# Performance work log

Hardware: AMD Instinct MI355X
Metric: run time of the kernel (lower is better)

## Reference

```python
import math
import jax, jax.numpy as jnp
import numpy as np

D_MODEL = 1024
N_HEADS = 16
D_K = 64


def setup_inputs() -> dict:
    key = jax.random.key(0)
    ks = jax.random.split(key, 12)
    N, T = 4, 2048
    hd = N_HEADS * D_K
    s_in = 1.0 / math.sqrt(D_MODEL)
    s_hd = 1.0 / math.sqrt(hd)
    return {
        "x_k": jax.random.normal(ks[0], (N, T, D_MODEL), jnp.float32),
        "x_v": jax.random.normal(ks[1], (N, T, D_MODEL), jnp.float32),
        "x_q": jax.random.normal(ks[2], (N, T, D_MODEL), jnp.float32),
        "mask": jnp.ones((N, T), jnp.int32),
        "Wk": jax.random.normal(ks[3], (D_MODEL, hd), jnp.float32) * s_in,
        "bk": jax.random.normal(ks[4], (hd,), jnp.float32) * s_in,
        "Wv": jax.random.normal(ks[5], (D_MODEL, hd), jnp.float32) * s_in,
        "bv": jax.random.normal(ks[6], (hd,), jnp.float32) * s_in,
        "Wq": jax.random.normal(ks[7], (D_MODEL, hd), jnp.float32) * s_in,
        "bq": jax.random.normal(ks[8], (hd,), jnp.float32) * s_in,
        "Wf": jax.random.normal(ks[9], (hd, D_MODEL), jnp.float32) * s_hd,
        "bf": jax.random.normal(ks[10], (D_MODEL,), jnp.float32) * s_hd,
    }


def _split_heads(x):  # [N,T,H*D] -> [N,H,T,D]
    n, t, _ = x.shape
    return x.reshape(n, t, N_HEADS, D_K).transpose(0, 2, 1, 3)


def reference(x_k, x_v, x_q, mask, Wk, bk, Wv, bv, Wq, bq, Wf, bf):
    k = _split_heads(x_k @ Wk + bk)  # projected but (faithfully) unused in scores
    v = _split_heads(x_v @ Wv + bv)
    q = _split_heads(x_q @ Wq + bq)
    # NOTE: original code computes scores from q and v (not k) — reproduced faithfully.
    scores = jnp.einsum('nhid,nhjd->nhij', q, v) / math.sqrt(D_K)
    scores = jnp.where(mask[:, None, None, :] == 0, -jnp.inf, scores)
    weights = jax.nn.softmax(scores, axis=-1)
    A = jnp.einsum('nhij,nhjd->nhid', weights, v)  # [N,H,T,D]
    n, h, t, d = A.shape
    A = A.transpose(0, 2, 1, 3).reshape(n, t, h * d)
    return A @ Wf + bf
```

## Files before the change

### kernel.cpp

```cpp
#include <hip/hip_runtime.h>
#include <cstdint>
#include <type_traits>

typedef unsigned short u16;
typedef __attribute__((ext_vector_type(8))) short short8;
typedef __attribute__((ext_vector_type(4))) float f32x4;

#define DMODEL 1024
#define TSEQ   2048
#define NHEADS 16
#define DKH    64
#define NBATCH 4
#define MROWS  (NBATCH * TSEQ)

__device__ __forceinline__ u16 f2b(float f) {
  union { float f; unsigned int u; } c; c.f = f;
  unsigned int u = c.u;
  return (u16)((u + 0x7fffu + ((u >> 16) & 1u)) >> 16);
}

__device__ __forceinline__ void gl_lds16(const u16* g, u16* l) {
  __builtin_amdgcn_global_load_lds((const __attribute__((address_space(1))) void*)g,
                                   (__attribute__((address_space(3))) void*)l, 16, 0, 0);
}

__global__ void cvt_bf16(const float* __restrict__ in, u16* __restrict__ out) {
  int i = blockIdx.x * 256 + threadIdx.x;
  const float4* p = (const float4*)in + (long long)i * 2;
  float4 a = p[0], b = p[1];
  union { u16 s[8]; uint4 v; } pk;
  pk.s[0] = f2b(a.x); pk.s[1] = f2b(a.y); pk.s[2] = f2b(a.z); pk.s[3] = f2b(a.w);
  pk.s[4] = f2b(b.x); pk.s[5] = f2b(b.y); pk.s[6] = f2b(b.z); pk.s[7] = f2b(b.w);
  ((uint4*)out)[i] = pk.v;
}

__global__ void transpose_cvt(const float* __restrict__ in, u16* __restrict__ out) {
  __shared__ float t[32][33];
  int bx = blockIdx.x * 32, by = blockIdx.y * 32;
  int tx = threadIdx.x, ty = threadIdx.y;
  #pragma unroll
  for (int i = ty; i < 32; i += 8)
    t[i][tx] = in[(by + i) * DMODEL + bx + tx];
  __syncthreads();
  #pragma unroll
  for (int i = ty; i < 32; i += 8)
    out[(bx + i) * DMODEL + by + tx] = f2b(t[tx][i]);
}

__global__ void transpose_v(const u16* __restrict__ Vb, u16* __restrict__ VbT) {
  __shared__ u16 tl[64 * 66];
  int tb = blockIdx.x, h = blockIdx.y, nb = blockIdx.z;
  int tx = threadIdx.x, ty = threadIdx.y;
  long long src = (long long)(nb * TSEQ + tb * 64) * DMODEL + h * DKH;
  #pragma unroll
  for (int r = ty; r < 64; r += 4)
    tl[r * 66 + tx] = Vb[src + (long long)r * DMODEL + tx];
  __syncthreads();
  long long dst = (long long)((nb * NHEADS + h) * DKH) * TSEQ + tb * 64;
  #pragma unroll
  for (int r = ty; r < 64; r += 4)
    VbT[dst + (long long)r * TSEQ + tx] = tl[tx * 66 + r];
}

template <typename CT>
__global__ __launch_bounds__(256, 2)
void gemm_bias(const u16* __restrict__ A, const u16* __restrict__ Bt,
               const float* __restrict__ bias, CT* __restrict__ C) {
  __shared__ u16 As[128 * 64];
  __shared__ u16 Bs[128 * 64];

  const int tid  = threadIdx.x;
  const int bm   = blockIdx.x, bn = blockIdx.y;
  const int wv   = tid >> 6, lane = tid & 63;
  const int wm   = wv >> 1, wn = wv & 1;
  const int l15  = lane & 15, quad = lane >> 4;
  const int srow = lane >> 3;
  const int gch  = (lane & 7) ^ srow;

  f32x4 acc[4][4];
  #pragma unroll
  for (int i = 0; i < 4; ++i)
    #pragma unroll
    for (int j = 0; j < 4; ++j)
      acc[i][j] = (f32x4){0.f, 0.f, 0.f, 0.f};

  const u16* Ag = A  + (long long)(bm * 128) * DMODEL;
  const u16* Bg = Bt + (long long)(bn * 128) * DMODEL;

  for (int k0 = 0; k0 < DMODEL; k0 += 64) {
    __syncthreads();
    #pragma unroll
    for (int j = 0; j < 4; ++j) {
      int rb = wv * 32 + j * 8;
      gl_lds16(Ag + (long long)(rb + srow) * DMODEL + k0 + gch * 8, As + rb * 64);
      gl_lds16(Bg + (long long)(rb + srow) * DMODEL + k0 + gch * 8, Bs + rb * 64);
    }
    __syncthreads();
    #pragma unroll
    for (int ks = 0; ks < 2; ++ks) {
      short8 af[4], bf_[4];
      #pragma unroll
      for (int mi = 0; mi < 4; ++mi) {
        int r = wm * 64 + mi * 16 + l15;
        af[mi] = *(const short8*)(As + r * 64 + (((ks * 4 + quad) ^ (r & 7)) * 8));
      }
      #pragma unroll
      for (int ni = 0; ni < 4; ++ni) {
        int r = wn * 64 + ni * 16 + l15;
        bf_[ni] = *(const short8*)(Bs + r * 64 + (((ks * 4 + quad) ^ (r & 7)) * 8));
      }
      #pragma unroll
      for (int mi = 0; mi < 4; ++mi)
        #pragma unroll
        for (int ni = 0; ni < 4; ++ni)
          acc[mi][ni] = __builtin_amdgcn_mfma_f32_16x16x32_bf16(af[mi], bf_[ni], acc[mi][ni], 0, 0, 0);
    }
  }

  #pragma unroll
  for (int ni = 0; ni < 4; ++ni) {
    int col = bn * 128 + wn * 64 + ni * 16 + l15;
    float bvf = bias[col];
    #pragma unroll
    for (int mi = 0; mi < 4; ++mi) {
      int row0 = bm * 128 + wm * 64 + mi * 16 + quad * 4;
      #pragma unroll
      for (int r = 0; r < 4; ++r) {
        float val = acc[mi][ni][r] + bvf;
        long long idx = (long long)(row0 + r) * DMODEL + col;
        if constexpr (std::is_same_v<CT, float>) C[idx] = val;
        else                                     C[idx] = f2b(val);
      }
    }
  }
}

__global__ __launch_bounds__(256, 4)
void attn_kernel(const u16* __restrict__ Qb, const u16* __restrict__ Vb,
                 const u16* __restrict__ VbT, const int* __restrict__ mask,
                 u16* __restrict__ Ab) {
  __shared__ u16 Vs[64 * 64];
  __shared__ u16 Vts[64 * 64];
  __shared__ u16 Ps[4 * 32 * 72];
  __shared__ float Msf[64];

  const int tid  = threadIdx.x;
  const int qblk = blockIdx.x, h = blockIdx.y, nb = blockIdx.z;
  const int wv   = tid >> 6, lane = tid & 63;
  const int l15  = lane & 15, quad = lane >> 4;
  const int srow = lane >> 3, gch = (lane & 7) ^ srow;

  const int q0 = qblk * 128 + wv * 32;
  const long long rowbase = (long long)nb * TSEQ;
  const long long hd = (long long)((nb * NHEADS + h) * DKH);
  u16* psb = Ps + wv * 32 * 72;

  short8 qf[2][2];
  #pragma unroll
  for (int mi = 0; mi < 2; ++mi)
    #pragma unroll
    for (int ks = 0; ks < 2; ++ks)
      qf[mi][ks] = *(const short8*)(Qb + (rowbase + q0 + mi * 16 + l15) * DMODEL
                                    + h * DKH + ks * 32 + quad * 8);

  f32x4 of[2][4];
  #pragma unroll
  for (int mi = 0; mi < 2; ++mi)
    #pragma unroll
    for (int dt = 0; dt < 4; ++dt)
      of[mi][dt] = (f32x4){0.f, 0.f, 0.f, 0.f};
  float lsum[2] = {0.f, 0.f};

  const float SC = 0.125f * 1.44269504f;

  for (int vb = 0; vb < TSEQ / 64; ++vb) {
    __syncthreads();
    #pragma unroll
    for (int j = 0; j < 2; ++j) {
      int rb = wv * 16 + j * 8;
      gl_lds16(Vb  + (rowbase + vb * 64 + rb + srow) * DMODEL + h * DKH + gch * 8, Vs  + rb * 64);
      gl_lds16(VbT + (hd + rb + srow) * TSEQ + vb * 64 + gch * 8,                  Vts + rb * 64);
    }
    if (tid < 64) Msf[tid] = mask[nb * TSEQ + vb * 64 + tid] ? 0.f : -INFINITY;
    __syncthreads();

    f32x4 st[2][4];
    #pragma unroll
    for (int mi = 0; mi < 2; ++mi)
      #pragma unroll
      for (int tt = 0; tt < 4; ++tt)
        st[mi][tt] = (f32x4){0.f, 0.f, 0.f, 0.f};
    #pragma unroll
    for (int tt = 0; tt < 4; ++tt) {
      int r = tt * 16 + l15;
      #pragma unroll
      for (int ks = 0; ks < 2; ++ks) {
        short8 vf = *(const short8*)(Vs + r * 64 + (((ks * 4 + quad) ^ (l15 & 7)) * 8));
        #pragma unroll
        for (int mi = 0; mi < 2; ++mi)
          st[mi][tt] = __builtin_amdgcn_mfma_f32_16x16x32_bf16(vf, qf[mi][ks], st[mi][tt], 0, 0, 0);
      }
    }

    f32x4 msk[4];
    #pragma unroll
    for (int tt = 0; tt < 4; ++tt)
      msk[tt] = *(const f32x4*)(Msf + tt * 16 + quad * 4);
    #pragma unroll
    for (int mi = 0; mi < 2; ++mi) {
      float ls = 0.f;
      #pragma unroll
      for (int tt = 0; tt < 4; ++tt) {
        float p0 = __builtin_amdgcn_exp2f(__builtin_fmaf(st[mi][tt][0], SC, msk[tt][0]));
        float p1 = __builtin_amdgcn_exp2f(__builtin_fmaf(st[mi][tt][1], SC, msk[tt][1]));
        float p2 = __builtin_amdgcn_exp2f(__builtin_fmaf(st[mi][tt][2], SC, msk[tt][2]));
        float p3 = __builtin_amdgcn_exp2f(__builtin_fmaf(st[mi][tt][3], SC, msk[tt][3]));
        ls += (p0 + p1) + (p2 + p3);
        uint2 pk;
        pk.x = (unsigned)f2b(p0) | ((unsigned)f2b(p1) << 16);
        pk.y = (unsigned)f2b(p2) | ((unsigned)f2b(p3) << 16);
        *(uint2*)(psb + (mi * 16 + l15) * 72 + tt * 16 + quad * 4) = pk;
      }
      lsum[mi] += ls;
    }

    #pragma unroll
    for (int kc = 0; kc < 2; ++kc) {
      short8 pf[2];
      #pragma unroll
      for (int mi = 0; mi < 2; ++mi)
        pf[mi] = *(const short8*)(psb + (mi * 16 + l15) * 72 + kc * 32 + quad * 8);
      #pragma unroll
      for (int dt = 0; dt < 4; ++dt) {
        int r = dt * 16 + l15;
        short8 vtf = *(const short8*)(Vts + r * 64 + (((kc * 4 + quad) ^ (l15 & 7)) * 8));
        #pragma unroll
        for (int mi = 0; mi < 2; ++mi)
          of[mi][dt] = __builtin_amdgcn_mfma_f32_16x16x32_bf16(vtf, pf[mi], of[mi][dt], 0, 0, 0);
      }
    }
  }

  #pragma unroll
  for (int mi = 0; mi < 2; ++mi) {
    float l = lsum[mi];
    l += __shfl_xor(l, 16, 64);
    l += __shfl_xor(l, 32, 64);
    float inv = 1.0f / l;
    long long row = rowbase + q0 + mi * 16 + l15;
    #pragma unroll
    for (int dt = 0; dt < 4; ++dt) {
      union { u16 s[4]; uint2 v; } o;
      #pragma unroll
      for (int r = 0; r < 4; ++r) o.s[r] = f2b(of[mi][dt][r] * inv);
      *(uint2*)(Ab + row * DMODEL + h * DKH + dt * 16 + quad * 4) = o.v;
    }
  }
}

extern "C" void kernel_launch(void* const* d_in, const int* in_sizes, int n_in,
                              void* d_out, int out_size, void* d_ws, size_t ws_size,
                              hipStream_t stream) {
  const float* x_v  = (const float*)d_in[1];
  const float* x_q  = (const float*)d_in[2];
  const int*   mask = (const int*)d_in[3];
  const float* Wv   = (const float*)d_in[6];
  const float* bv   = (const float*)d_in[7];
  const float* Wq   = (const float*)d_in[8];
  const float* bq   = (const float*)d_in[9];
  const float* Wf   = (const float*)d_in[10];
  const float* bfp  = (const float*)d_in[11];

  char* w = (char*)d_ws;
  u16* WqT = (u16*)(w + 0);
  u16* WvT = (u16*)(w + (2ll << 20));
  u16* WfT = (u16*)(w + (4ll << 20));
  u16* Xq  = (u16*)(w + (6ll << 20));
  u16* Xv  = (u16*)(w + (22ll << 20));
  u16* Qb  = (u16*)(w + (38ll << 20));
  u16* Vb  = (u16*)(w + (54ll << 20));
  u16* VbT = (u16*)(w + (70ll << 20));
  u16* Ab  = Xq;

  dim3 tb(32, 8), tg(32, 32);
  transpose_cvt<<<tg, tb, 0, stream>>>(Wq, WqT);
  transpose_cvt<<<tg, tb, 0, stream>>>(Wv, WvT);
  transpose_cvt<<<tg, tb, 0, stream>>>(Wf, WfT);

  cvt_bf16<<<MROWS * DMODEL / 8 / 256, 256, 0, stream>>>(x_q, Xq);
  cvt_bf16<<<MROWS * DMODEL / 8 / 256, 256, 0, stream>>>(x_v, Xv);

  dim3 gg(MROWS / 128, DMODEL / 128);
  gemm_bias<u16><<<gg, 256, 0, stream>>>(Xq, WqT, bq, Qb);
  gemm_bias<u16><<<gg, 256, 0, stream>>>(Xv, WvT, bv, Vb);

  transpose_v<<<dim3(TSEQ / 64, NHEADS, NBATCH), dim3(64, 4), 0, stream>>>(Vb, VbT);

  attn_kernel<<<dim3(TSEQ / 128, NHEADS, NBATCH), 256, 0, stream>>>(Qb, Vb, VbT, mask, Ab);

  gemm_bias<float><<<gg, 256, 0, stream>>>(Ab, WfT, bfp, (float*)d_out);
}
```

Baseline: 376.7 us.

## Switch PV and output GEMM to fp16, fold softmax scale into Q, merge Q/V GEMMs

Merges the Q and V projection GEMMs into one launch using a z-dimension selector, and folds the softmax scale and log2e into the Q projection epilogue. The attention P·V product, the transposed V and the attention output now use fp16 with packed round-toward-zero conversions, and the output GEMM runs on fp16 MFMA. The row sum uses fdot2, and the mask add is skipped when a wave-wide check finds no masked keys in the tile. These changes cut per-element conversion and masking ALU work and launch count. In exchange, Q and V are now rounded to bf16 after scaling, fp16 can overflow for large values, and there are more precision differences to manage.

```diff
diff --git a/kernel.cpp b/kernel.cpp
--- a/kernel.cpp
+++ b/kernel.cpp
@@ -4,6 +4,8 @@
 
 typedef unsigned short u16;
 typedef __attribute__((ext_vector_type(8))) short short8;
+typedef __attribute__((ext_vector_type(8))) __fp16 half8;
+typedef __attribute__((ext_vector_type(2))) __fp16 half2v;
 typedef __attribute__((ext_vector_type(4))) float f32x4;
 
 #define DMODEL 1024
@@ -12,11 +14,25 @@
 #define DKH    64
 #define NBATCH 4
 #define MROWS  (NBATCH * TSEQ)
-
+#define QSCALE 0.18033688011f
+
+__device__ __forceinline__ float b2f(u16 u) {
+  union { unsigned int u; float f; } c; c.u = ((unsigned int)u) << 16; return c.f;
+}
 __device__ __forceinline__ u16 f2b(float f) {
   union { float f; unsigned int u; } c; c.f = f;
   unsigned int u = c.u;
   return (u16)((u + 0x7fffu + ((u >> 16) & 1u)) >> 16);
+}
+__device__ __forceinline__ half2v pkrtz(float a, float b) {
+  return __builtin_amdgcn_cvt_pkrtz(a, b);
+}
+__device__ __forceinline__ unsigned h2u(half2v h) {
+  unsigned u; __builtin_memcpy(&u, &h, 4); return u;
+}
+__device__ __forceinline__ u16 f2h(float f) {
+  half2v h = pkrtz(f, 0.f);
+  u16 u; __builtin_memcpy(&u, &h, 2); return u;
 }
 
 __device__ __forceinline__ void gl_lds16(const u16* g, u16* l) {
@@ -34,6 +50,7 @@
   ((uint4*)out)[i] = pk.v;
 }
 
+template <bool F16>
 __global__ void transpose_cvt(const float* __restrict__ in, u16* __restrict__ out) {
   __shared__ float t[32][33];
   int bx = blockIdx.x * 32, by = blockIdx.y * 32;
@@ -44,7 +61,7 @@
   __syncthreads();
   #pragma unroll
   for (int i = ty; i < 32; i += 8)
-    out[(bx + i) * DMODEL + by + tx] = f2b(t[tx][i]);
+    out[(bx + i) * DMODEL + by + tx] = F16 ? f2h(t[tx][i]) : f2b(t[tx][i]);
 }
 
 __global__ void transpose_v(const u16* __restrict__ Vb, u16* __restrict__ VbT) {
@@ -59,23 +76,20 @@
   long long dst = (long long)((nb * NHEADS + h) * DKH) * TSEQ + tb * 64;
   #pragma unroll
   for (int r = ty; r < 64; r += 4)
-    VbT[dst + (long long)r * TSEQ + tx] = tl[tx * 66 + r];
-}
-
-template <typename CT>
-__global__ __launch_bounds__(256, 2)
-void gemm_bias(const u16* __restrict__ A, const u16* __restrict__ Bt,
-               const float* __restrict__ bias, CT* __restrict__ C) {
-  __shared__ u16 As[128 * 64];
-  __shared__ u16 Bs[128 * 64];
-
+    VbT[dst + (long long)r * TSEQ + tx] = f2h(b2f(tl[tx * 66 + r]));
+}
+
+template <bool F16, typename CT>
+__device__ __forceinline__ void gemm_core(
+    u16* As, u16* Bs,
+    const u16* __restrict__ A, const u16* __restrict__ Bt,
+    const float* __restrict__ bias, CT* __restrict__ C,
+    const int bm, const int bn, const float osc) {
   const int tid  = threadIdx.x;
-  const int bm   = blockIdx.x, bn = blockIdx.y;
   const int wv   = tid >> 6, lane = tid & 63;
   const int wm   = wv >> 1, wn = wv & 1;
   const int l15  = lane & 15, quad = lane >> 4;
-  const int srow = lane >> 3;
-  const int gch  = (lane & 7) ^ srow;
+  const int srow = lane >> 3, gch = (lane & 7) ^ srow;
 
   f32x4 acc[4][4];
   #pragma unroll
@@ -98,22 +112,22 @@
     __syncthreads();
     #pragma unroll
     for (int ks = 0; ks < 2; ++ks) {
-      short8 af[4], bf_[4];
       #pragma unroll
       for (int mi = 0; mi < 4; ++mi) {
-        int r = wm * 64 + mi * 16 + l15;
-        af[mi] = *(const short8*)(As + r * 64 + (((ks * 4 + quad) ^ (r & 7)) * 8));
-      }
-      #pragma unroll
-      for (int ni = 0; ni < 4; ++ni) {
-        int r = wn * 64 + ni * 16 + l15;
-        bf_[ni] = *(const short8*)(Bs + r * 64 + (((ks * 4 + quad) ^ (r & 7)) * 8));
-      }
-      #pragma unroll
-      for (int mi = 0; mi < 4; ++mi)
+        int ra = wm * 64 + mi * 16 + l15;
+        const u16* pa = As + ra * 64 + (((ks * 4 + quad) ^ (ra & 7)) * 8);
         #pragma unroll
-        for (int ni = 0; ni < 4; ++ni)
-          acc[mi][ni] = __builtin_amdgcn_mfma_f32_16x16x32_bf16(af[mi], bf_[ni], acc[mi][ni], 0, 0, 0);
+        for (int ni = 0; ni < 4; ++ni) {
+          int rb = wn * 64 + ni * 16 + l15;
+          const u16* pb = Bs + rb * 64 + (((ks * 4 + quad) ^ (rb & 7)) * 8);
+          if constexpr (F16)
+            acc[mi][ni] = __builtin_amdgcn_mfma_f32_16x16x32_f16(
+                *(const half8*)pa, *(const half8*)pb, acc[mi][ni], 0, 0, 0);
+          else
+            acc[mi][ni] = __builtin_amdgcn_mfma_f32_16x16x32_bf16(
+                *(const short8*)pa, *(const short8*)pb, acc[mi][ni], 0, 0, 0);
+        }
+      }
     }
   }
 
@@ -126,7 +140,7 @@
       int row0 = bm * 128 + wm * 64 + mi * 16 + quad * 4;
       #pragma unroll
       for (int r = 0; r < 4; ++r) {
-        float val = acc[mi][ni][r] + bvf;
+        float val = (acc[mi][ni][r] + bvf) * osc;
         long long idx = (long long)(row0 + r) * DMODEL + col;
         if constexpr (std::is_same_v<CT, float>) C[idx] = val;
         else                                     C[idx] = f2b(val);
@@ -136,8 +150,29 @@
 }
 
 __global__ __launch_bounds__(256, 4)
+void gemm_qv(const u16* __restrict__ Xq, const u16* __restrict__ Xv,
+             const u16* __restrict__ WqT, const u16* __restrict__ WvT,
+             const float* __restrict__ bq, const float* __restrict__ bv,
+             u16* __restrict__ Qb, u16* __restrict__ Vb) {
+  __shared__ u16 As[128 * 64];
+  __shared__ u16 Bs[128 * 64];
+  const bool isq = (blockIdx.z == 0);
+  gemm_core<false, u16>(As, Bs, isq ? Xq : Xv, isq ? WqT : WvT,
+                        isq ? bq : bv, isq ? Qb : Vb,
+                        blockIdx.x, blockIdx.y, isq ? QSCALE : 1.0f);
+}
+
+__global__ __launch_bounds__(256, 2)
+void gemm_out(const u16* __restrict__ A, const u16* __restrict__ Bt,
+              const float* __restrict__ bias, float* __restrict__ C) {
+  __shared__ u16 As[128 * 64];
+  __shared__ u16 Bs[128 * 64];
+  gemm_core<true, float>(As, Bs, A, Bt, bias, C, blockIdx.x, blockIdx.y, 1.0f);
+}
+
+__global__ __launch_bounds__(256, 4)
 void attn_kernel(const u16* __restrict__ Qb, const u16* __restrict__ Vb,
-                 const u16* __restrict__ VbT, const int* __restrict__ mask,
+                 const u16* __restrict__ VbTh, const int* __restrict__ mask,
                  u16* __restrict__ Ab) {
   __shared__ u16 Vs[64 * 64];
   __shared__ u16 Vts[64 * 64];
@@ -170,18 +205,19 @@
     for (int dt = 0; dt < 4; ++dt)
       of[mi][dt] = (f32x4){0.f, 0.f, 0.f, 0.f};
   float lsum[2] = {0.f, 0.f};
-
-  const float SC = 0.125f * 1.44269504f;
+  const half2v one2 = {(__fp16)1.f, (__fp16)1.f};
 
   for (int vb = 0; vb < TSEQ / 64; ++vb) {
     __syncthreads();
     #pragma unroll
     for (int j = 0; j < 2; ++j) {
       int rb = wv * 16 + j * 8;
-      gl_lds16(Vb  + (rowbase + vb * 64 + rb + srow) * DMODEL + h * DKH + gch * 8, Vs  + rb * 64);
-      gl_lds16(VbT + (hd + rb + srow) * TSEQ + vb * 64 + gch * 8,                  Vts + rb * 64);
-    }
-    if (tid < 64) Msf[tid] = mask[nb * TSEQ + vb * 64 + tid] ? 0.f : -INFINITY;
+      gl_lds16(Vb   + (rowbase + vb * 64 + rb + srow) * DMODEL + h * DKH + gch * 8, Vs  + rb * 64);
+      gl_lds16(VbTh + (hd + rb + srow) * TSEQ + vb * 64 + gch * 8,                  Vts + rb * 64);
+    }
+    int mv = mask[nb * TSEQ + vb * 64 + lane];
+    if (tid < 64) Msf[tid] = mv ? 0.f : -INFINITY;
+    const bool slowm = __any(mv == 0);
     __syncthreads();
 
     f32x4 st[2][4];
@@ -203,40 +239,47 @@
     }
 
     f32x4 msk[4];
-    #pragma unroll
-    for (int tt = 0; tt < 4; ++tt)
-      msk[tt] = *(const f32x4*)(Msf + tt * 16 + quad * 4);
+    if (slowm) {
+      #pragma unroll
+      for (int tt = 0; tt < 4; ++tt)
+        msk[tt] = *(const f32x4*)(Msf + tt * 16 + quad * 4);
+    }
     #pragma unroll
     for (int mi = 0; mi < 2; ++mi) {
-      float ls = 0.f;
       #pragma unroll
       for (int tt = 0; tt < 4; ++tt) {
-        float p0 = __builtin_amdgcn_exp2f(__builtin_fmaf(st[mi][tt][0], SC, msk[tt][0]));
-        float p1 = __builtin_amdgcn_exp2f(__builtin_fmaf(st[mi][tt][1], SC, msk[tt][1]));
-        float p2 = __builtin_amdgcn_exp2f(__builtin_fmaf(st[mi][tt][2], SC, msk[tt][2]));
-        float p3 = __builtin_amdgcn_exp2f(__builtin_fmaf(st[mi][tt][3], SC, msk[tt][3]));
-        ls += (p0 + p1) + (p2 + p3);
-        uint2 pk;
-        pk.x = (unsigned)f2b(p0) | ((unsigned)f2b(p1) << 16);
-        pk.y = (unsigned)f2b(p2) | ((unsigned)f2b(p3) << 16);
+        float a0 = st[mi][tt][0], a1 = st[mi][tt][1];
+        float a2 = st[mi][tt][2], a3 = st[mi][tt][3];
+        if (slowm) { a0 += msk[tt][0]; a1 += msk[tt][1]; a2 += msk[tt][2]; a3 += msk[tt][3]; }
+        float p0 = __builtin_amdgcn_exp2f(a0);
+        float p1 = __builtin_amdgcn_exp2f(a1);
+        float p2 = __builtin_amdgcn_exp2f(a2);
+        float p3 = __builtin_amdgcn_exp2f(a3);
+        half2v h01 = pkrtz(p0, p1), h23 = pkrtz(p2, p3);
+#if __has_builtin(__builtin_amdgcn_fdot2)
+        lsum[mi] = __builtin_amdgcn_fdot2(h01, one2, lsum[mi], false);
+        lsum[mi] = __builtin_amdgcn_fdot2(h23, one2, lsum[mi], false);
+#else
+        lsum[mi] += (p0 + p1) + (p2 + p3);
+#endif
+        uint2 pk; pk.x = h2u(h01); pk.y = h2u(h23);
         *(uint2*)(psb + (mi * 16 + l15) * 72 + tt * 16 + quad * 4) = pk;
       }
-      lsum[mi] += ls;
     }
 
     #pragma unroll
     for (int kc = 0; kc < 2; ++kc) {
-      short8 pf[2];
+      half8 pf[2];
       #pragma unroll
       for (int mi = 0; mi < 2; ++mi)
-        pf[mi] = *(const short8*)(psb + (mi * 16 + l15) * 72 + kc * 32 + quad * 8);
+        pf[mi] = *(const half8*)(psb + (mi * 16 + l15) * 72 + kc * 32 + quad * 8);
       #pragma unroll
       for (int dt = 0; dt < 4; ++dt) {
         int r = dt * 16 + l15;
-        short8 vtf = *(const short8*)(Vts + r * 64 + (((kc * 4 + quad) ^ (l15 & 7)) * 8));
+        half8 vtf = *(const half8*)(Vts + r * 64 + (((kc * 4 + quad) ^ (l15 & 7)) * 8));
         #pragma unroll
         for (int mi = 0; mi < 2; ++mi)
-          of[mi][dt] = __builtin_amdgcn_mfma_f32_16x16x32_bf16(vtf, pf[mi], of[mi][dt], 0, 0, 0);
+          of[mi][dt] = __builtin_amdgcn_mfma_f32_16x16x32_f16(vtf, pf[mi], of[mi][dt], 0, 0, 0);
       }
     }
   }
@@ -250,10 +293,10 @@
     long long row = rowbase + q0 + mi * 16 + l15;
     #pragma unroll
     for (int dt = 0; dt < 4; ++dt) {
-      union { u16 s[4]; uint2 v; } o;
-      #pragma unroll
-      for (int r = 0; r < 4; ++r) o.s[r] = f2b(of[mi][dt][r] * inv);
-      *(uint2*)(Ab + row * DMODEL + h * DKH + dt * 16 + quad * 4) = o.v;
+      uint2 o;
+      o.x = h2u(pkrtz(of[mi][dt][0] * inv, of[mi][dt][1] * inv));
+      o.y = h2u(pkrtz(of[mi][dt][2] * inv, of[mi][dt][3] * inv));
+      *(uint2*)(Ab + row * DMODEL + h * DKH + dt * 16 + quad * 4) = o;
     }
   }
 }
@@ -272,31 +315,30 @@
   const float* bfp  = (const float*)d_in[11];
 
   char* w = (char*)d_ws;
-  u16* WqT = (u16*)(w + 0);
-  u16* WvT = (u16*)(w + (2ll << 20));
-  u16* WfT = (u16*)(w + (4ll << 20));
-  u16* Xq  = (u16*)(w + (6ll << 20));
-  u16* Xv  = (u16*)(w + (22ll << 20));
-  u16* Qb  = (u16*)(w + (38ll << 20));
-  u16* Vb  = (u16*)(w + (54ll << 20));
-  u16* VbT = (u16*)(w + (70ll << 20));
-  u16* Ab  = Xq;
+  u16* WqT  = (u16*)(w + 0);
+  u16* WvT  = (u16*)(w + (2ll << 20));
+  u16* WfT  = (u16*)(w + (4ll << 20));
+  u16* Xq   = (u16*)(w + (6ll << 20));
+  u16* Xv   = (u16*)(w + (22ll << 20));
+  u16* Qb   = (u16*)(w + (38ll << 20));
+  u16* Vb   = (u16*)(w + (54ll << 20));
+  u16* VbTh = (u16*)(w + (70ll << 20));
+  u16* Ab   = Xq;
 
   dim3 tb(32, 8), tg(32, 32);
-  transpose_cvt<<<tg, tb, 0, stream>>>(Wq, WqT);
-  transpose_cvt<<<tg, tb, 0, stream>>>(Wv, WvT);
-  transpose_cvt<<<tg, tb, 0, stream>>>(Wf, WfT);
+  transpose_cvt<false><<<tg, tb, 0, stream>>>(Wq, WqT);
+  transpose_cvt<false><<<tg, tb, 0, stream>>>(Wv, WvT);
+  transpose_cvt<true ><<<tg, tb, 0, stream>>>(Wf, WfT);
 
   cvt_bf16<<<MROWS * DMODEL / 8 / 256, 256, 0, stream>>>(x_q, Xq);
   cvt_bf16<<<MROWS * DMODEL / 8 / 256, 256, 0, stream>>>(x_v, Xv);
 
-  dim3 gg(MROWS / 128, DMODEL / 128);
-  gemm_bias<u16><<<gg, 256, 0, stream>>>(Xq, WqT, bq, Qb);
-  gemm_bias<u16><<<gg, 256, 0, stream>>>(Xv, WvT, bv, Vb);
-
-  transpose_v<<<dim3(TSEQ / 64, NHEADS, NBATCH), dim3(64, 4), 0, stream>>>(Vb, VbT);
-
-  attn_kernel<<<dim3(TSEQ / 128, NHEADS, NBATCH), 256, 0, stream>>>(Qb, Vb, VbT, mask, Ab);
-
-  gemm_bias<float><<<gg, 256, 0, stream>>>(Ab, WfT, bfp, (float*)d_out);
-}
+  gemm_qv<<<dim3(MROWS / 128, DMODEL / 128, 2), 256, 0, stream>>>(
+      Xq, Xv, WqT, WvT, bq, bv, Qb, Vb);
+
+  transpose_v<<<dim3(TSEQ / 64, NHEADS, NBATCH), dim3(64, 4), 0, stream>>>(Vb, VbTh);
+
+  attn_kernel<<<dim3(TSEQ / 128, NHEADS, NBATCH), 256, 0, stream>>>(Qb, Vb, VbTh, mask, Ab);
+
+  gemm_out<<<dim3(MROWS / 128, DMODEL / 128), 256, 0, stream>>>(Ab, WfT, bfp, (float*)d_out);
+}
```

New measurement: 323.4 us. 1.17x faster.
